# Performance work log

Hardware: AMD Instinct MI355X
Metric: run time of the kernel (lower is better)

## Reference

```python
import jax, jax.numpy as jnp
import numpy as np
from jax import lax

K = 3
J = 3
NU = 0.001
ALPHA = 0.1
DIM = 1792      # wrn50_2 feature dim
SCALE = 64      # hard-coded self.scale
N_CENTERS = SCALE * SCALE  # gamma_c = 1


def setup_inputs() -> dict:
    key = jax.random.key(0)
    k1, k2, k3, k4 = jax.random.split(key, 4)
    B = 4
    sample = jax.random.normal(k1, (B, DIM, SCALE, SCALE), dtype=jnp.float32)
    # CoordConv2d(dim, dim//gamma_d, 1): 1x1 conv over [features, xx, yy]
    W = jax.random.normal(k2, (DIM, DIM + 2), dtype=jnp.float32) * 0.02
    b = jnp.zeros((DIM,), dtype=jnp.float32)
    # C: [c, n_centers] after transpose in __init__
    C = jax.random.normal(k3, (DIM, N_CENTERS), dtype=jnp.float32) * 0.02
    r = 1e-5 * jnp.ones((1,), dtype=jnp.float32)
    return {"sample": sample, "W": W, "b": b, "C": C, "r": r}


def _coordconv_1x1(sample, W, b):
    B, Cin, H, Wd = sample.shape
    yy = jnp.linspace(-1.0, 1.0, H, dtype=sample.dtype)
    xx = jnp.linspace(-1.0, 1.0, Wd, dtype=sample.dtype)
    xx_g = jnp.broadcast_to(xx[None, None, None, :], (B, 1, H, Wd))
    yy_g = jnp.broadcast_to(yy[None, None, :, None], (B, 1, H, Wd))
    x = jnp.concatenate([sample, xx_g, yy_g], axis=1)  # [B, Cin+2, H, W]
    # 1x1 conv == channel matmul
    return jnp.einsum('bihw,oi->bohw', x, W) + b[None, :, None, None]


def reference(sample, W, b, C, r):
    B, _, H, Wd = sample.shape
    phi = _coordconv_1x1(sample, W, b)                 # [B, c, H, W]
    phi_p = phi.reshape(B, phi.shape[1], H * Wd).transpose(0, 2, 1)  # [B, HW, c]

    feat2 = jnp.sum(phi_p * phi_p, axis=2, keepdims=True)   # [B, HW, 1]
    cent2 = jnp.sum(C * C, axis=0)[None, None, :]            # [1, 1, N]
    dist2 = feat2 + cent2 - 2.0 * jnp.einsum('bnc,ck->bnk', phi_p, C)  # [B, HW, N]

    # --- score path (inference) ---
    d = jnp.sqrt(jnp.maximum(dist2, 0.0))
    dk = -lax.top_k(-d, K)[0]                     # K smallest, ascending
    w = jax.nn.softmax(-dk, axis=-1)              # softmin
    s = w[:, :, 0] * dk[:, :, 0]                  # [B, HW]
    score = s.reshape(B, H, Wd)[:, None]          # [B, 1, H, W]

    # --- soft-boundary loss (training) ---
    dkj = -lax.top_k(-dist2, K + J)[0]            # K+J smallest squared dists
    r2 = r ** 2
    sc_att = dkj[:, :, :K] - r2
    L_att = (1.0 / NU) * jnp.mean(jnp.maximum(sc_att, 0.0))
    sc_rep = r2 - dkj[:, :, J:]
    L_rep = (1.0 / NU) * jnp.mean(jnp.maximum(sc_rep - ALPHA, 0.0))
    loss = L_att + L_rep
    return loss, score
```

## Files before the change

### kernel.cpp

```cpp
#include <hip/hip_runtime.h>
#include <hip/hip_bf16.h>

using v8s = __attribute__((ext_vector_type(8))) short;
using v4f = __attribute__((ext_vector_type(4))) float;

#define DIMC 1792
#define NROW 16384
#define NCEN 4096
#define BIGF 3.0e38f

#define GL2LDS16(g, l) __builtin_amdgcn_global_load_lds(                      \
    (const __attribute__((address_space(1))) void*)(g),                       \
    (__attribute__((address_space(3))) void*)(l), 16, 0, 0)

__device__ __forceinline__ void ce(float& a, float& b) {
  float lo = fminf(a, b), hi = fmaxf(a, b); a = lo; b = hi;
}

template<int MASK>
__device__ __forceinline__ void merge6(float s[6]) {
  float p[6];
#pragma unroll
  for (int i = 0; i < 6; ++i) p[i] = __shfl_xor(s[i], MASK);
  float t[6];
#pragma unroll
  for (int i = 0; i < 6; ++i) t[i] = fminf(s[i], p[5 - i]);
  ce(t[0], t[3]); ce(t[1], t[4]); ce(t[2], t[5]);
  ce(t[0], t[2]); ce(t[0], t[1]); ce(t[1], t[2]);
  ce(t[3], t[5]); ce(t[3], t[4]); ce(t[4], t[5]);
#pragma unroll
  for (int i = 0; i < 6; ++i) s[i] = t[i];
}

__global__ void transpose_cvt(const float* __restrict__ in, __hip_bfloat16* __restrict__ out) {
  __shared__ float tile[32][33];
  const int tx = threadIdx.x, ty = threadIdx.y;
  const size_t zoff = (size_t)blockIdx.z * DIMC * NCEN;
  const float* inb = in + zoff;
  __hip_bfloat16* outb = out + zoff;
  const int r0 = blockIdx.y * 32, c0 = blockIdx.x * 32;
#pragma unroll
  for (int j = 0; j < 4; ++j) {
    int rr = ty + j * 8;
    tile[rr][tx] = inb[(size_t)(r0 + rr) * 4096 + c0 + tx];
  }
  __syncthreads();
#pragma unroll
  for (int j = 0; j < 4; ++j) {
    int rr = ty + j * 8;
    outb[(size_t)(c0 + rr) * DIMC + r0 + tx] = __float2bfloat16(tile[tx][rr]);
  }
}

__global__ void w_convert(const float* __restrict__ W, __hip_bfloat16* __restrict__ Wb) {
  int idx = blockIdx.x * 256 + threadIdx.x;
  int o = idx / DIMC, i = idx - o * DIMC;
  Wb[idx] = __float2bfloat16(W[(size_t)o * 1794 + i]);
}

__global__ void rowsq(const __hip_bfloat16* __restrict__ src, float* __restrict__ dst) {
  const int row = blockIdx.x, t = threadIdx.x;
  float s = 0.f;
  if (t < 224) {
    const uint4 v = *(const uint4*)((const unsigned short*)src + (size_t)row * DIMC + t * 8);
    unsigned int u0 = v.x, u1 = v.y, u2 = v.z, u3 = v.w;
    float a, b;
    a = __uint_as_float(u0 << 16); b = __uint_as_float(u0 & 0xFFFF0000u); s += a * a + b * b;
    a = __uint_as_float(u1 << 16); b = __uint_as_float(u1 & 0xFFFF0000u); s += a * a + b * b;
    a = __uint_as_float(u2 << 16); b = __uint_as_float(u2 & 0xFFFF0000u); s += a * a + b * b;
    a = __uint_as_float(u3 << 16); b = __uint_as_float(u3 & 0xFFFF0000u); s += a * a + b * b;
  }
  __shared__ float red[256];
  red[t] = s; __syncthreads();
  for (int off = 128; off > 0; off >>= 1) { if (t < off) red[t] += red[t + off]; __syncthreads(); }
  if (t == 0) dst[row] = red[0];
}

__global__ __launch_bounds__(256) void gemm_phi(
    const __hip_bfloat16* __restrict__ Xb, const __hip_bfloat16* __restrict__ Wb,
    const float* __restrict__ W, const float* __restrict__ bvec,
    __hip_bfloat16* __restrict__ phib) {
  __shared__ __align__(16) __hip_bfloat16 As[128 * 32];
  __shared__ __align__(16) __hip_bfloat16 Bs[128 * 32];
  const int t = threadIdx.x;
  const int l = t & 63, w = t >> 6, wr = w >> 1, wc = w & 1;
  const int n0 = blockIdx.x * 128, o0 = blockIdx.y * 128;
  const int rowS = t >> 2, gS = (t & 3) ^ ((rowS >> 1) & 3);
  const unsigned short* aP0 = (const unsigned short*)Xb + (size_t)(n0 + rowS) * DIMC + gS * 8;
  const unsigned short* aP1 = aP0 + (size_t)64 * DIMC;
  const unsigned short* bP0 = (const unsigned short*)Wb + (size_t)(o0 + rowS) * DIMC + gS * 8;
  const unsigned short* bP1 = bP0 + (size_t)64 * DIMC;
  char* ldsA0 = (char*)As + w * 1024;
  char* ldsA1 = (char*)As + 4096 + w * 1024;
  char* ldsB0 = (char*)Bs + w * 1024;
  char* ldsB1 = (char*)Bs + 4096 + w * 1024;
  const int col = l & 15, g = l >> 4, pr = g ^ ((col >> 1) & 3);
  int offA[4], offB[4];
#pragma unroll
  for (int i = 0; i < 4; ++i) {
    offA[i] = (wr * 64 + i * 16 + col) * 32 + pr * 8;
    offB[i] = (wc * 64 + i * 16 + col) * 32 + pr * 8;
  }
  v4f acc[4][4] = {};
  for (int kt = 0; kt < DIMC; kt += 32) {
    __syncthreads();
    GL2LDS16(aP0 + kt, ldsA0);
    GL2LDS16(aP1 + kt, ldsA1);
    GL2LDS16(bP0 + kt, ldsB0);
    GL2LDS16(bP1 + kt, ldsB1);
    __syncthreads();
    v8s af[4], bf[4];
#pragma unroll
    for (int i = 0; i < 4; ++i) af[i] = *(const v8s*)((const unsigned short*)As + offA[i]);
#pragma unroll
    for (int i = 0; i < 4; ++i) bf[i] = *(const v8s*)((const unsigned short*)Bs + offB[i]);
#pragma unroll
    for (int mi = 0; mi < 4; ++mi)
#pragma unroll
      for (int ni = 0; ni < 4; ++ni)
        acc[mi][ni] = __builtin_amdgcn_mfma_f32_16x16x32_bf16(af[mi], bf[ni], acc[mi][ni], 0, 0, 0);
  }
#pragma unroll
  for (int ni = 0; ni < 4; ++ni) {
    const int o = o0 + wc * 64 + ni * 16 + col;
    const float bo = bvec[o];
    const float wx = W[(size_t)o * 1794 + 1792];
    const float wy = W[(size_t)o * 1794 + 1793];
#pragma unroll
    for (int mi = 0; mi < 4; ++mi) {
#pragma unroll
      for (int j = 0; j < 4; ++j) {
        const int n = n0 + wr * 64 + mi * 16 + g * 4 + j;
        const int wi = n & 63, hi = (n >> 6) & 63;
        const float xxv = -1.f + (2.f / 63.f) * wi;
        const float yyv = -1.f + (2.f / 63.f) * hi;
        float v = acc[mi][ni][j] + bo + wx * xxv + wy * yyv;
        phib[(size_t)n * DIMC + o] = __float2bfloat16(v);
      }
    }
  }
}

__global__ __launch_bounds__(256) void gemm_dist(
    const __hip_bfloat16* __restrict__ phib, const __hip_bfloat16* __restrict__ Ct,
    const float* __restrict__ feat2, const float* __restrict__ cent2,
    float* __restrict__ cand) {
  __shared__ __align__(16) __hip_bfloat16 As[128 * 32];
  __shared__ __align__(16) __hip_bfloat16 Bs[128 * 32];
  const int t = threadIdx.x;
  const int l = t & 63, w = t >> 6, wr = w >> 1, wc = w & 1;
  const int n0 = blockIdx.x * 128, o0 = blockIdx.y * 128;
  const int rowS = t >> 2, gS = (t & 3) ^ ((rowS >> 1) & 3);
  const unsigned short* aP0 = (const unsigned short*)phib + (size_t)(n0 + rowS) * DIMC + gS * 8;
  const unsigned short* aP1 = aP0 + (size_t)64 * DIMC;
  const unsigned short* bP0 = (const unsigned short*)Ct + (size_t)(o0 + rowS) * DIMC + gS * 8;
  const unsigned short* bP1 = bP0 + (size_t)64 * DIMC;
  char* ldsA0 = (char*)As + w * 1024;
  char* ldsA1 = (char*)As + 4096 + w * 1024;
  char* ldsB0 = (char*)Bs + w * 1024;
  char* ldsB1 = (char*)Bs + 4096 + w * 1024;
  const int col = l & 15, g = l >> 4, pr = g ^ ((col >> 1) & 3);
  int offA[4], offB[4];
#pragma unroll
  for (int i = 0; i < 4; ++i) {
    offA[i] = (wr * 64 + i * 16 + col) * 32 + pr * 8;
    offB[i] = (wc * 64 + i * 16 + col) * 32 + pr * 8;
  }
  v4f acc[4][4] = {};
  for (int kt = 0; kt < DIMC; kt += 32) {
    __syncthreads();
    GL2LDS16(aP0 + kt, ldsA0);
    GL2LDS16(aP1 + kt, ldsA1);
    GL2LDS16(bP0 + kt, ldsB0);
    GL2LDS16(bP1 + kt, ldsB1);
    __syncthreads();
    v8s af[4], bf[4];
#pragma unroll
    for (int i = 0; i < 4; ++i) af[i] = *(const v8s*)((const unsigned short*)As + offA[i]);
#pragma unroll
    for (int i = 0; i < 4; ++i) bf[i] = *(const v8s*)((const unsigned short*)Bs + offB[i]);
#pragma unroll
    for (int mi = 0; mi < 4; ++mi)
#pragma unroll
      for (int ni = 0; ni < 4; ++ni)
        acc[mi][ni] = __builtin_amdgcn_mfma_f32_16x16x32_bf16(af[mi], bf[ni], acc[mi][ni], 0, 0, 0);
  }
  float c2v0 = cent2[o0 + wc * 64 + 0 * 16 + col];
  float c2v1 = cent2[o0 + wc * 64 + 1 * 16 + col];
  float c2v2 = cent2[o0 + wc * 64 + 2 * 16 + col];
  float c2v3 = cent2[o0 + wc * 64 + 3 * 16 + col];
  const int cg = blockIdx.y * 2 + wc;
#pragma unroll
  for (int mi = 0; mi < 4; ++mi) {
#pragma unroll
    for (int j = 0; j < 4; ++j) {
      const int n = n0 + wr * 64 + mi * 16 + g * 4 + j;
      const float f2 = feat2[n];
      float s[6];
      s[0] = f2 + c2v0 - 2.f * acc[mi][0][j];
      s[1] = f2 + c2v1 - 2.f * acc[mi][1][j];
      s[2] = f2 + c2v2 - 2.f * acc[mi][2][j];
      s[3] = f2 + c2v3 - 2.f * acc[mi][3][j];
      ce(s[0], s[1]); ce(s[2], s[3]); ce(s[0], s[2]); ce(s[1], s[3]); ce(s[1], s[2]);
      s[4] = BIGF; s[5] = BIGF;
      merge6<1>(s); merge6<2>(s); merge6<4>(s); merge6<8>(s);
      if (col == 0) {
        float* cp = cand + ((size_t)n * 64 + cg) * 6;
#pragma unroll
        for (int r = 0; r < 6; ++r) cp[r] = s[r];
      }
    }
  }
}

__global__ void finalize(const float* __restrict__ cand, const float* __restrict__ rvec,
                         float* __restrict__ rowloss, float* __restrict__ score) {
  const int n = blockIdx.x, l = threadIdx.x;
  const float* cp = cand + ((size_t)n * 64 + l) * 6;
  float s[6];
#pragma unroll
  for (int i = 0; i < 6; ++i) s[i] = cp[i];
  merge6<1>(s); merge6<2>(s); merge6<4>(s); merge6<8>(s); merge6<16>(s); merge6<32>(s);
  if (l == 0) {
    const float r2 = rvec[0] * rvec[0];
    float att = 0.f, rep = 0.f;
#pragma unroll
    for (int i = 0; i < 3; ++i) att += fmaxf(s[i] - r2, 0.f);
#pragma unroll
    for (int i = 3; i < 6; ++i) rep += fmaxf(r2 - s[i] - 0.1f, 0.f);
    rowloss[n] = att + rep;
    float dk0 = sqrtf(fmaxf(s[0], 0.f));
    float dk1 = sqrtf(fmaxf(s[1], 0.f));
    float dk2 = sqrtf(fmaxf(s[2], 0.f));
    float e1 = expf(dk0 - dk1), e2 = expf(dk0 - dk2);
    score[n] = dk0 / (1.f + e1 + e2);
  }
}

__global__ void reduce_loss(const float* __restrict__ rowloss, float* __restrict__ out) {
  const int t = threadIdx.x;
  float s = 0.f;
  for (int i = t; i < NROW; i += 256) s += rowloss[i];
  __shared__ float red[256];
  red[t] = s; __syncthreads();
  for (int off = 128; off > 0; off >>= 1) { if (t < off) red[t] += red[t + off]; __syncthreads(); }
  if (t == 0) out[0] = red[0] / (0.001f * 49152.f);
}

extern "C" void kernel_launch(void* const* d_in, const int* in_sizes, int n_in,
                              void* d_out, int out_size, void* d_ws, size_t ws_size,
                              hipStream_t stream) {
  const float* sample = (const float*)d_in[0];
  const float* W      = (const float*)d_in[1];
  const float* bvec   = (const float*)d_in[2];
  const float* C      = (const float*)d_in[3];
  const float* rv     = (const float*)d_in[4];
  float* out = (float*)d_out;

  char* p = (char*)d_ws;
  auto take = [&](size_t bytes) { char* q = p; p += (bytes + 255) & ~(size_t)255; return q; };
  __hip_bfloat16* Xb   = (__hip_bfloat16*)take((size_t)NROW * DIMC * 2);
  __hip_bfloat16* Wb   = (__hip_bfloat16*)take((size_t)DIMC * DIMC * 2);
  __hip_bfloat16* Ct   = (__hip_bfloat16*)take((size_t)NCEN * DIMC * 2);
  __hip_bfloat16* phib = (__hip_bfloat16*)take((size_t)NROW * DIMC * 2);
  float* feat2   = (float*)take((size_t)NROW * 4);
  float* cent2   = (float*)take((size_t)NCEN * 4);
  float* cand    = (float*)take((size_t)NROW * 64 * 6 * 4);
  float* rowloss = (float*)take((size_t)NROW * 4);

  transpose_cvt<<<dim3(128, 56, 4), dim3(32, 8), 0, stream>>>(sample, Xb);
  transpose_cvt<<<dim3(128, 56, 1), dim3(32, 8), 0, stream>>>(C, Ct);
  w_convert<<<dim3(12544), dim3(256), 0, stream>>>(W, Wb);
  rowsq<<<dim3(NCEN), dim3(256), 0, stream>>>(Ct, cent2);
  gemm_phi<<<dim3(128, 14), dim3(256), 0, stream>>>(Xb, Wb, W, bvec, phib);
  rowsq<<<dim3(NROW), dim3(256), 0, stream>>>(phib, feat2);
  gemm_dist<<<dim3(128, 32), dim3(256), 0, stream>>>(phib, Ct, feat2, cent2, cand);
  finalize<<<dim3(NROW), dim3(64), 0, stream>>>(cand, rv, rowloss, out + 1);
  reduce_loss<<<dim3(1), dim3(256), 0, stream>>>(rowloss, out);
}
```

Baseline: 728.4 us.

## Triple-buffer LDS K-tiles in both GEMMs with one fenced barrier per step

The single-buffered K loop in both gemm_phi and gemm_dist becomes a three-stage ring of LDS buffers. Each step issues the global→LDS loads for the tile two steps ahead, computes on the current tile, then waits with vmcnt(4) and one barrier. This lets global load latency overlap MFMA work and removes one of the two barriers per K step. In exchange, LDS per block grows to 48KB, which may reduce how many blocks fit on each CU, and correctness relies on the hand-written vmcnt counts.

```diff
diff --git a/kernel.cpp b/kernel.cpp
--- a/kernel.cpp
+++ b/kernel.cpp
@@ -12,6 +12,13 @@
 #define GL2LDS16(g, l) __builtin_amdgcn_global_load_lds(                      \
     (const __attribute__((address_space(1))) void*)(g),                       \
     (__attribute__((address_space(3))) void*)(l), 16, 0, 0)
+
+#define FENCE_BAR(N) do {                                                     \
+    asm volatile("s_waitcnt vmcnt(" #N ")" ::: "memory");                     \
+    __builtin_amdgcn_sched_barrier(0);                                        \
+    __builtin_amdgcn_s_barrier();                                             \
+    __builtin_amdgcn_sched_barrier(0);                                        \
+  } while (0)
 
 __device__ __forceinline__ void ce(float& a, float& b) {
   float lo = fminf(a, b), hi = fmaxf(a, b); a = lo; b = hi;
@@ -80,8 +87,7 @@
     const __hip_bfloat16* __restrict__ Xb, const __hip_bfloat16* __restrict__ Wb,
     const float* __restrict__ W, const float* __restrict__ bvec,
     __hip_bfloat16* __restrict__ phib) {
-  __shared__ __align__(16) __hip_bfloat16 As[128 * 32];
-  __shared__ __align__(16) __hip_bfloat16 Bs[128 * 32];
+  __shared__ __align__(16) char L[49152];
   const int t = threadIdx.x;
   const int l = t & 63, w = t >> 6, wr = w >> 1, wc = w & 1;
   const int n0 = blockIdx.x * 128, o0 = blockIdx.y * 128;
@@ -90,36 +96,46 @@
   const unsigned short* aP1 = aP0 + (size_t)64 * DIMC;
   const unsigned short* bP0 = (const unsigned short*)Wb + (size_t)(o0 + rowS) * DIMC + gS * 8;
   const unsigned short* bP1 = bP0 + (size_t)64 * DIMC;
-  char* ldsA0 = (char*)As + w * 1024;
-  char* ldsA1 = (char*)As + 4096 + w * 1024;
-  char* ldsB0 = (char*)Bs + w * 1024;
-  char* ldsB1 = (char*)Bs + 4096 + w * 1024;
+  char* A0 = L;         char* A1 = L + 8192;  char* A2 = L + 16384;
+  char* B0 = L + 24576; char* B1 = L + 32768; char* B2 = L + 40960;
+  const int woff = w * 1024;
   const int col = l & 15, g = l >> 4, pr = g ^ ((col >> 1) & 3);
   int offA[4], offB[4];
 #pragma unroll
   for (int i = 0; i < 4; ++i) {
-    offA[i] = (wr * 64 + i * 16 + col) * 32 + pr * 8;
-    offB[i] = (wc * 64 + i * 16 + col) * 32 + pr * 8;
+    offA[i] = ((wr * 64 + i * 16 + col) * 32 + pr * 8) * 2;
+    offB[i] = ((wc * 64 + i * 16 + col) * 32 + pr * 8) * 2;
   }
   v4f acc[4][4] = {};
-  for (int kt = 0; kt < DIMC; kt += 32) {
-    __syncthreads();
-    GL2LDS16(aP0 + kt, ldsA0);
-    GL2LDS16(aP1 + kt, ldsA1);
-    GL2LDS16(bP0 + kt, ldsB0);
-    GL2LDS16(bP1 + kt, ldsB1);
-    __syncthreads();
+  auto stage = [&](int ke, char* sA, char* sB) {
+    GL2LDS16(aP0 + ke, sA + woff);
+    GL2LDS16(aP1 + ke, sA + 4096 + woff);
+    GL2LDS16(bP0 + ke, sB + woff);
+    GL2LDS16(bP1 + ke, sB + 4096 + woff);
+  };
+  auto compute = [&](const char* rA, const char* rB) {
     v8s af[4], bf[4];
 #pragma unroll
-    for (int i = 0; i < 4; ++i) af[i] = *(const v8s*)((const unsigned short*)As + offA[i]);
-#pragma unroll
-    for (int i = 0; i < 4; ++i) bf[i] = *(const v8s*)((const unsigned short*)Bs + offB[i]);
+    for (int i = 0; i < 4; ++i) af[i] = *(const v8s*)(rA + offA[i]);
+#pragma unroll
+    for (int i = 0; i < 4; ++i) bf[i] = *(const v8s*)(rB + offB[i]);
 #pragma unroll
     for (int mi = 0; mi < 4; ++mi)
 #pragma unroll
       for (int ni = 0; ni < 4; ++ni)
         acc[mi][ni] = __builtin_amdgcn_mfma_f32_16x16x32_bf16(af[mi], bf[ni], acc[mi][ni], 0, 0, 0);
-  }
+  };
+  stage(0, A0, B0);
+  stage(32, A1, B1);
+  FENCE_BAR(4);
+  for (int k3 = 0; k3 < 54; k3 += 3) {
+    stage((k3 + 2) * 32, A2, B2); compute(A0, B0); FENCE_BAR(4);
+    stage((k3 + 3) * 32, A0, B0); compute(A1, B1); FENCE_BAR(4);
+    stage((k3 + 4) * 32, A1, B1); compute(A2, B2); FENCE_BAR(4);
+  }
+  compute(A0, B0);
+  FENCE_BAR(0);
+  compute(A1, B1);
 #pragma unroll
   for (int ni = 0; ni < 4; ++ni) {
     const int o = o0 + wc * 64 + ni * 16 + col;
@@ -145,8 +161,7 @@
     const __hip_bfloat16* __restrict__ phib, const __hip_bfloat16* __restrict__ Ct,
     const float* __restrict__ feat2, const float* __restrict__ cent2,
     float* __restrict__ cand) {
-  __shared__ __align__(16) __hip_bfloat16 As[128 * 32];
-  __shared__ __align__(16) __hip_bfloat16 Bs[128 * 32];
+  __shared__ __align__(16) char L[49152];
   const int t = threadIdx.x;
   const int l = t & 63, w = t >> 6, wr = w >> 1, wc = w & 1;
   const int n0 = blockIdx.x * 128, o0 = blockIdx.y * 128;
@@ -155,36 +170,46 @@
   const unsigned short* aP1 = aP0 + (size_t)64 * DIMC;
   const unsigned short* bP0 = (const unsigned short*)Ct + (size_t)(o0 + rowS) * DIMC + gS * 8;
   const unsigned short* bP1 = bP0 + (size_t)64 * DIMC;
-  char* ldsA0 = (char*)As + w * 1024;
-  char* ldsA1 = (char*)As + 4096 + w * 1024;
-  char* ldsB0 = (char*)Bs + w * 1024;
-  char* ldsB1 = (char*)Bs + 4096 + w * 1024;
+  char* A0 = L;         char* A1 = L + 8192;  char* A2 = L + 16384;
+  char* B0 = L + 24576; char* B1 = L + 32768; char* B2 = L + 40960;
+  const int woff = w * 1024;
   const int col = l & 15, g = l >> 4, pr = g ^ ((col >> 1) & 3);
   int offA[4], offB[4];
 #pragma unroll
   for (int i = 0; i < 4; ++i) {
-    offA[i] = (wr * 64 + i * 16 + col) * 32 + pr * 8;
-    offB[i] = (wc * 64 + i * 16 + col) * 32 + pr * 8;
+    offA[i] = ((wr * 64 + i * 16 + col) * 32 + pr * 8) * 2;
+    offB[i] = ((wc * 64 + i * 16 + col) * 32 + pr * 8) * 2;
   }
   v4f acc[4][4] = {};
-  for (int kt = 0; kt < DIMC; kt += 32) {
-    __syncthreads();
-    GL2LDS16(aP0 + kt, ldsA0);
-    GL2LDS16(aP1 + kt, ldsA1);
-    GL2LDS16(bP0 + kt, ldsB0);
-    GL2LDS16(bP1 + kt, ldsB1);
-    __syncthreads();
+  auto stage = [&](int ke, char* sA, char* sB) {
+    GL2LDS16(aP0 + ke, sA + woff);
+    GL2LDS16(aP1 + ke, sA + 4096 + woff);
+    GL2LDS16(bP0 + ke, sB + woff);
+    GL2LDS16(bP1 + ke, sB + 4096 + woff);
+  };
+  auto compute = [&](const char* rA, const char* rB) {
     v8s af[4], bf[4];
 #pragma unroll
-    for (int i = 0; i < 4; ++i) af[i] = *(const v8s*)((const unsigned short*)As + offA[i]);
-#pragma unroll
-    for (int i = 0; i < 4; ++i) bf[i] = *(const v8s*)((const unsigned short*)Bs + offB[i]);
+    for (int i = 0; i < 4; ++i) af[i] = *(const v8s*)(rA + offA[i]);
+#pragma unroll
+    for (int i = 0; i < 4; ++i) bf[i] = *(const v8s*)(rB + offB[i]);
 #pragma unroll
     for (int mi = 0; mi < 4; ++mi)
 #pragma unroll
       for (int ni = 0; ni < 4; ++ni)
         acc[mi][ni] = __builtin_amdgcn_mfma_f32_16x16x32_bf16(af[mi], bf[ni], acc[mi][ni], 0, 0, 0);
-  }
+  };
+  stage(0, A0, B0);
+  stage(32, A1, B1);
+  FENCE_BAR(4);
+  for (int k3 = 0; k3 < 54; k3 += 3) {
+    stage((k3 + 2) * 32, A2, B2); compute(A0, B0); FENCE_BAR(4);
+    stage((k3 + 3) * 32, A0, B0); compute(A1, B1); FENCE_BAR(4);
+    stage((k3 + 4) * 32, A1, B1); compute(A2, B2); FENCE_BAR(4);
+  }
+  compute(A0, B0);
+  FENCE_BAR(0);
+  compute(A1, B1);
   float c2v0 = cent2[o0 + wc * 64 + 0 * 16 + col];
   float c2v1 = cent2[o0 + wc * 64 + 1 * 16 + col];
   float c2v2 = cent2[o0 + wc * 64 + 2 * 16 + col];
```

Result: no change. 714.8 us (-1.9%).

## Enlarge GEMM tiles to 256x256 with triple-buffered async LDS pipeline

Applied to the files above, without the earlier changes.

Both MFMA GEMMs now use 256x256 block tiles with 8 waves, each wave computing 128x64. K-tiles are staged through a three-deep LDS ring via global_load_lds, with vmcnt-based fences so loads overlap compute, replacing the two-barrier-per-step, single-buffer loop. MFMA sections get raised scheduling priority. The goal is to hide global load latency and raise reuse per byte loaded, at the cost of 96KB dynamic LDS, higher register pressure and fewer blocks.

```diff
diff --git a/kernel.cpp b/kernel.cpp
--- a/kernel.cpp
+++ b/kernel.cpp
@@ -12,6 +12,13 @@
 #define GL2LDS16(g, l) __builtin_amdgcn_global_load_lds(                      \
     (const __attribute__((address_space(1))) void*)(g),                       \
     (__attribute__((address_space(3))) void*)(l), 16, 0, 0)
+
+#define FENCE_BAR(N) do {                                                     \
+    asm volatile("s_waitcnt vmcnt(" #N ")" ::: "memory");                     \
+    __builtin_amdgcn_sched_barrier(0);                                        \
+    __builtin_amdgcn_s_barrier();                                             \
+    __builtin_amdgcn_sched_barrier(0);                                        \
+  } while (0)
 
 __device__ __forceinline__ void ce(float& a, float& b) {
   float lo = fminf(a, b), hi = fmaxf(a, b); a = lo; b = hi;
@@ -76,61 +83,87 @@
   if (t == 0) dst[row] = red[0];
 }
 
-__global__ __launch_bounds__(256) void gemm_phi(
+
+#define GEMM_PRE(APTR, BPTR)                                                  \
+  extern __shared__ __align__(16) char L[];                                   \
+  const int t = threadIdx.x;                                                  \
+  const int l = t & 63, w = t >> 6, wm = w >> 2, wn = w & 3;                  \
+  const int n0 = blockIdx.x * 256, o0 = blockIdx.y * 256;                     \
+  const int rowS = t >> 2, gS = (t & 3) ^ ((rowS >> 1) & 3);                  \
+  const unsigned short* aP0 = (const unsigned short*)(APTR) + (size_t)(n0 + rowS) * DIMC + gS * 8; \
+  const unsigned short* aP1 = aP0 + (size_t)128 * DIMC;                       \
+  const unsigned short* bP0 = (const unsigned short*)(BPTR) + (size_t)(o0 + rowS) * DIMC + gS * 8; \
+  const unsigned short* bP1 = bP0 + (size_t)128 * DIMC;                       \
+  char* A0 = L;          char* B0 = L + 16384;                                \
+  char* A1 = L + 32768;  char* B1 = L + 49152;                                \
+  char* A2 = L + 65536;  char* B2 = L + 81920;                                \
+  const int woff = w * 1024;                                                  \
+  const int col = l & 15, g = l >> 4, pr = g ^ ((col >> 1) & 3);              \
+  int offA[8], offB[4];                                                       \
+  _Pragma("unroll")                                                           \
+  for (int i = 0; i < 8; ++i) offA[i] = ((wm * 128 + i * 16 + col) * 32 + pr * 8) * 2; \
+  _Pragma("unroll")                                                           \
+  for (int i = 0; i < 4; ++i) offB[i] = ((wn * 64 + i * 16 + col) * 32 + pr * 8) * 2;  \
+  v4f acc[8][4] = {};                                                         \
+  auto stage = [&](int ke, char* sA, char* sB) {                              \
+    GL2LDS16(aP0 + ke, sA + woff);                                            \
+    GL2LDS16(aP1 + ke, sA + 8192 + woff);                                     \
+    GL2LDS16(bP0 + ke, sB + woff);                                            \
+    GL2LDS16(bP1 + ke, sB + 8192 + woff);                                     \
+  };                                                                          \
+  auto compute = [&](const char* rA, const char* rB) {                        \
+    v8s af[4], bf[4];                                                         \
+    _Pragma("unroll")                                                         \
+    for (int i = 0; i < 4; ++i) af[i] = *(const v8s*)(rA + offA[i]);          \
+    _Pragma("unroll")                                                         \
+    for (int i = 0; i < 4; ++i) bf[i] = *(const v8s*)(rB + offB[i]);          \
+    __builtin_amdgcn_s_setprio(1);                                            \
+    _Pragma("unroll")                                                         \
+    for (int mi = 0; mi < 4; ++mi)                                            \
+      _Pragma("unroll")                                                       \
+      for (int ni = 0; ni < 4; ++ni)                                          \
+        acc[mi][ni] = __builtin_amdgcn_mfma_f32_16x16x32_bf16(af[mi], bf[ni], acc[mi][ni], 0, 0, 0); \
+    __builtin_amdgcn_s_setprio(0);                                            \
+    __builtin_amdgcn_sched_barrier(0);                                        \
+    v8s a2[4];                                                                \
+    _Pragma("unroll")                                                         \
+    for (int i = 0; i < 4; ++i) a2[i] = *(const v8s*)(rA + offA[4 + i]);      \
+    __builtin_amdgcn_s_setprio(1);                                            \
+    _Pragma("unroll")                                                         \
+    for (int mi = 0; mi < 4; ++mi)                                            \
+      _Pragma("unroll")                                                       \
+      for (int ni = 0; ni < 4; ++ni)                                          \
+        acc[4 + mi][ni] = __builtin_amdgcn_mfma_f32_16x16x32_bf16(a2[mi], bf[ni], acc[4 + mi][ni], 0, 0, 0); \
+    __builtin_amdgcn_s_setprio(0);                                            \
+  };                                                                          \
+  stage(0, A0, B0);                                                           \
+  stage(32, A1, B1);                                                          \
+  FENCE_BAR(4);                                                               \
+  for (int k3 = 0; k3 < 54; k3 += 3) {         \
+    stage((k3 + 2) * 32, A2, B2); compute(A0, B0); FENCE_BAR(4);              \
+    stage((k3 + 3) * 32, A0, B0); compute(A1, B1); FENCE_BAR(4);              \
+    stage((k3 + 4) * 32, A1, B1); compute(A2, B2); FENCE_BAR(4);              \
+  }                                                                           \
+  compute(A0, B0);                                               \
+  FENCE_BAR(0);                                     \
+  compute(A1, B1);
+
+__global__ __launch_bounds__(512, 2) void gemm_phi(
     const __hip_bfloat16* __restrict__ Xb, const __hip_bfloat16* __restrict__ Wb,
     const float* __restrict__ W, const float* __restrict__ bvec,
     __hip_bfloat16* __restrict__ phib) {
-  __shared__ __align__(16) __hip_bfloat16 As[128 * 32];
-  __shared__ __align__(16) __hip_bfloat16 Bs[128 * 32];
-  const int t = threadIdx.x;
-  const int l = t & 63, w = t >> 6, wr = w >> 1, wc = w & 1;
-  const int n0 = blockIdx.x * 128, o0 = blockIdx.y * 128;
-  const int rowS = t >> 2, gS = (t & 3) ^ ((rowS >> 1) & 3);
-  const unsigned short* aP0 = (const unsigned short*)Xb + (size_t)(n0 + rowS) * DIMC + gS * 8;
-  const unsigned short* aP1 = aP0 + (size_t)64 * DIMC;
-  const unsigned short* bP0 = (const unsigned short*)Wb + (size_t)(o0 + rowS) * DIMC + gS * 8;
-  const unsigned short* bP1 = bP0 + (size_t)64 * DIMC;
-  char* ldsA0 = (char*)As + w * 1024;
-  char* ldsA1 = (char*)As + 4096 + w * 1024;
-  char* ldsB0 = (char*)Bs + w * 1024;
-  char* ldsB1 = (char*)Bs + 4096 + w * 1024;
-  const int col = l & 15, g = l >> 4, pr = g ^ ((col >> 1) & 3);
-  int offA[4], offB[4];
-#pragma unroll
-  for (int i = 0; i < 4; ++i) {
-    offA[i] = (wr * 64 + i * 16 + col) * 32 + pr * 8;
-    offB[i] = (wc * 64 + i * 16 + col) * 32 + pr * 8;
-  }
-  v4f acc[4][4] = {};
-  for (int kt = 0; kt < DIMC; kt += 32) {
-    __syncthreads();
-    GL2LDS16(aP0 + kt, ldsA0);
-    GL2LDS16(aP1 + kt, ldsA1);
-    GL2LDS16(bP0 + kt, ldsB0);
-    GL2LDS16(bP1 + kt, ldsB1);
-    __syncthreads();
-    v8s af[4], bf[4];
-#pragma unroll
-    for (int i = 0; i < 4; ++i) af[i] = *(const v8s*)((const unsigned short*)As + offA[i]);
-#pragma unroll
-    for (int i = 0; i < 4; ++i) bf[i] = *(const v8s*)((const unsigned short*)Bs + offB[i]);
-#pragma unroll
-    for (int mi = 0; mi < 4; ++mi)
-#pragma unroll
-      for (int ni = 0; ni < 4; ++ni)
-        acc[mi][ni] = __builtin_amdgcn_mfma_f32_16x16x32_bf16(af[mi], bf[ni], acc[mi][ni], 0, 0, 0);
-  }
+  GEMM_PRE(Xb, Wb)
 #pragma unroll
   for (int ni = 0; ni < 4; ++ni) {
-    const int o = o0 + wc * 64 + ni * 16 + col;
+    const int o = o0 + wn * 64 + ni * 16 + col;
     const float bo = bvec[o];
     const float wx = W[(size_t)o * 1794 + 1792];
     const float wy = W[(size_t)o * 1794 + 1793];
 #pragma unroll
-    for (int mi = 0; mi < 4; ++mi) {
+    for (int mi = 0; mi < 8; ++mi) {
 #pragma unroll
       for (int j = 0; j < 4; ++j) {
-        const int n = n0 + wr * 64 + mi * 16 + g * 4 + j;
+        const int n = n0 + wm * 128 + mi * 16 + g * 4 + j;
         const int wi = n & 63, hi = (n >> 6) & 63;
         const float xxv = -1.f + (2.f / 63.f) * wi;
         const float yyv = -1.f + (2.f / 63.f) * hi;
@@ -141,66 +174,26 @@
   }
 }
 
-__global__ __launch_bounds__(256) void gemm_dist(
+__global__ __launch_bounds__(512, 2) void gemm_dist(
     const __hip_bfloat16* __restrict__ phib, const __hip_bfloat16* __restrict__ Ct,
     const float* __restrict__ feat2, const float* __restrict__ cent2,
     float* __restrict__ cand) {
-  __shared__ __align__(16) __hip_bfloat16 As[128 * 32];
-  __shared__ __align__(16) __hip_bfloat16 Bs[128 * 32];
-  const int t = threadIdx.x;
-  const int l = t & 63, w = t >> 6, wr = w >> 1, wc = w & 1;
-  const int n0 = blockIdx.x * 128, o0 = blockIdx.y * 128;
-  const int rowS = t >> 2, gS = (t & 3) ^ ((rowS >> 1) & 3);
-  const unsigned short* aP0 = (const unsigned short*)phib + (size_t)(n0 + rowS) * DIMC + gS * 8;
-  const unsigned short* aP1 = aP0 + (size_t)64 * DIMC;
-  const unsigned short* bP0 = (const unsigned short*)Ct + (size_t)(o0 + rowS) * DIMC + gS * 8;
-  const unsigned short* bP1 = bP0 + (size_t)64 * DIMC;
-  char* ldsA0 = (char*)As + w * 1024;
-  char* ldsA1 = (char*)As + 4096 + w * 1024;
-  char* ldsB0 = (char*)Bs + w * 1024;
-  char* ldsB1 = (char*)Bs + 4096 + w * 1024;
-  const int col = l & 15, g = l >> 4, pr = g ^ ((col >> 1) & 3);
-  int offA[4], offB[4];
-#pragma unroll
-  for (int i = 0; i < 4; ++i) {
-    offA[i] = (wr * 64 + i * 16 + col) * 32 + pr * 8;
-    offB[i] = (wc * 64 + i * 16 + col) * 32 + pr * 8;
-  }
-  v4f acc[4][4] = {};
-  for (int kt = 0; kt < DIMC; kt += 32) {
-    __syncthreads();
-    GL2LDS16(aP0 + kt, ldsA0);
-    GL2LDS16(aP1 + kt, ldsA1);
-    GL2LDS16(bP0 + kt, ldsB0);
-    GL2LDS16(bP1 + kt, ldsB1);
-    __syncthreads();
-    v8s af[4], bf[4];
-#pragma unroll
-    for (int i = 0; i < 4; ++i) af[i] = *(const v8s*)((const unsigned short*)As + offA[i]);
-#pragma unroll
-    for (int i = 0; i < 4; ++i) bf[i] = *(const v8s*)((const unsigned short*)Bs + offB[i]);
-#pragma unroll
-    for (int mi = 0; mi < 4; ++mi)
-#pragma unroll
-      for (int ni = 0; ni < 4; ++ni)
-        acc[mi][ni] = __builtin_amdgcn_mfma_f32_16x16x32_bf16(af[mi], bf[ni], acc[mi][ni], 0, 0, 0);
-  }
-  float c2v0 = cent2[o0 + wc * 64 + 0 * 16 + col];
-  float c2v1 = cent2[o0 + wc * 64 + 1 * 16 + col];
-  float c2v2 = cent2[o0 + wc * 64 + 2 * 16 + col];
-  float c2v3 = cent2[o0 + wc * 64 + 3 * 16 + col];
-  const int cg = blockIdx.y * 2 + wc;
-#pragma unroll
-  for (int mi = 0; mi < 4; ++mi) {
+  GEMM_PRE(phib, Ct)
+  float c2v[4];
+#pragma unroll
+  for (int ni = 0; ni < 4; ++ni) c2v[ni] = cent2[o0 + wn * 64 + ni * 16 + col];
+  const int cg = blockIdx.y * 4 + wn;
+#pragma unroll
+  for (int mi = 0; mi < 8; ++mi) {
 #pragma unroll
     for (int j = 0; j < 4; ++j) {
-      const int n = n0 + wr * 64 + mi * 16 + g * 4 + j;
+      const int n = n0 + wm * 128 + mi * 16 + g * 4 + j;
       const float f2 = feat2[n];
       float s[6];
-      s[0] = f2 + c2v0 - 2.f * acc[mi][0][j];
-      s[1] = f2 + c2v1 - 2.f * acc[mi][1][j];
-      s[2] = f2 + c2v2 - 2.f * acc[mi][2][j];
-      s[3] = f2 + c2v3 - 2.f * acc[mi][3][j];
+      s[0] = f2 + c2v[0] - 2.f * acc[mi][0][j];
+      s[1] = f2 + c2v[1] - 2.f * acc[mi][1][j];
+      s[2] = f2 + c2v[2] - 2.f * acc[mi][2][j];
+      s[3] = f2 + c2v[3] - 2.f * acc[mi][3][j];
       ce(s[0], s[1]); ce(s[2], s[3]); ce(s[0], s[2]); ce(s[1], s[3]); ce(s[1], s[2]);
       s[4] = BIGF; s[5] = BIGF;
       merge6<1>(s); merge6<2>(s); merge6<4>(s); merge6<8>(s);
@@ -268,13 +261,16 @@
   float* cand    = (float*)take((size_t)NROW * 64 * 6 * 4);
   float* rowloss = (float*)take((size_t)NROW * 4);
 
+  hipFuncSetAttribute((const void*)gemm_phi,  hipFuncAttributeMaxDynamicSharedMemorySize, 98304);
+  hipFuncSetAttribute((const void*)gemm_dist, hipFuncAttributeMaxDynamicSharedMemorySize, 98304);
+
   transpose_cvt<<<dim3(128, 56, 4), dim3(32, 8), 0, stream>>>(sample, Xb);
   transpose_cvt<<<dim3(128, 56, 1), dim3(32, 8), 0, stream>>>(C, Ct);
   w_convert<<<dim3(12544), dim3(256), 0, stream>>>(W, Wb);
   rowsq<<<dim3(NCEN), dim3(256), 0, stream>>>(Ct, cent2);
-  gemm_phi<<<dim3(128, 14), dim3(256), 0, stream>>>(Xb, Wb, W, bvec, phib);
+  gemm_phi<<<dim3(64, 7), dim3(512), 98304, stream>>>(Xb, Wb, W, bvec, phib);
   rowsq<<<dim3(NROW), dim3(256), 0, stream>>>(phib, feat2);
-  gemm_dist<<<dim3(128, 32), dim3(256), 0, stream>>>(phib, Ct, feat2, cent2, cand);
+  gemm_dist<<<dim3(64, 16), dim3(512), 98304, stream>>>(phib, Ct, feat2, cent2, cand);
   finalize<<<dim3(NROW), dim3(64), 0, stream>>>(cand, rv, rowloss, out + 1);
   reduce_loss<<<dim3(1), dim3(256), 0, stream>>>(rowloss, out);
 }
```

Result: faster. 653.5 us (-10.3%).
